# Kernel optimization log

Hardware: AMD Instinct MI355X
Metric: run time of the kernel (lower is better)

The kernel has to match this reference:

```python
import jax, jax.numpy as jnp
import numpy as np

N = 100000      # nodes
E = 1600000     # edges (avg degree 16)
F_IN = 128      # num_node_features
H = 128         # hidden_size
C = 64          # num_classes


def sage_conv(x, src, dst, W_l, W_r, b, num_nodes):
    """PyG SAGEConv (mean aggr): out = lin_l(mean_{j->i} x_j) + lin_r(x_i) + b."""
    msg = x[src]                                                  # [E, F] gather
    agg = jax.ops.segment_sum(msg, dst, num_segments=num_nodes)   # [N, F] scatter-add
    deg = jax.ops.segment_sum(jnp.ones((src.shape[0],), x.dtype), dst,
                              num_segments=num_nodes)             # [N]
    agg = agg / jnp.maximum(deg, 1.0)[:, None]                    # mean (safe for isolated nodes)
    return agg @ W_l + x @ W_r + b


def setup_inputs() -> dict:
    key = jax.random.key(0)
    ks = jax.random.split(key, 8)
    x = jax.random.normal(ks[0], (N, F_IN), dtype=jnp.float32)
    edge_index = jax.random.randint(ks[1], (2, E), 0, N, dtype=jnp.int32).astype(jnp.int64)
    W1_l = jax.random.normal(ks[2], (F_IN, H), dtype=jnp.float32) / np.float32(np.sqrt(F_IN))
    W1_r = jax.random.normal(ks[3], (F_IN, H), dtype=jnp.float32) / np.float32(np.sqrt(F_IN))
    b1 = jnp.zeros((H,), jnp.float32)
    W2_l = jax.random.normal(ks[4], (H, C), dtype=jnp.float32) / np.float32(np.sqrt(H))
    W2_r = jax.random.normal(ks[5], (H, C), dtype=jnp.float32) / np.float32(np.sqrt(H))
    b2 = jnp.zeros((C,), jnp.float32)
    return {"x": x, "edge_index": edge_index,
            "W1_l": W1_l, "W1_r": W1_r, "b1": b1,
            "W2_l": W2_l, "W2_r": W2_r, "b2": b2}


def reference(x, edge_index, W1_l, W1_r, b1, W2_l, W2_r, b2):
    src, dst = edge_index[0], edge_index[1]
    h = jax.nn.relu(sage_conv(x, src, dst, W1_l, W1_r, b1, N))   # dropout: eval mode => identity
    logits = sage_conv(h, src, dst, W2_l, W2_r, b2, N)
    return jax.nn.log_softmax(logits, axis=1)
```

## Files before the change

### kernel.cpp

```cpp
#include <hip/hip_runtime.h>

#define Nn 100000
#define Ee 1600000
#define FIN 128
#define HID 128
#define CLS 64
#define NB 196
#define BCAP 9216

typedef unsigned short ushort_t;
typedef unsigned char uchar_t;
typedef unsigned int uint_t;
typedef __attribute__((ext_vector_type(8))) short bf16x8;
typedef __attribute__((ext_vector_type(4))) float f32x4;
typedef __attribute__((ext_vector_type(2))) float f32x2;

__device__ __forceinline__ ushort_t f2bf(float f) {
    uint_t u = __float_as_uint(f);
    return (ushort_t)((u + 0x7fffu + ((u >> 16) & 1u)) >> 16);
}
__device__ __forceinline__ float bflo(uint_t u) { return __uint_as_float(u << 16); }
__device__ __forceinline__ float bfhi(uint_t u) { return __uint_as_float(u & 0xffff0000u); }


__global__ __launch_bounds__(1024) void k_front(const int* __restrict__ src,
                                                const int* __restrict__ dst,
                                                int* __restrict__ bcur,
                                                uint2* __restrict__ bedge,
                                                const float* __restrict__ x,
                                                ushort_t* __restrict__ xb,
                                                uint_t* __restrict__ xq,
                                                const float* __restrict__ W1l,
                                                const float* __restrict__ W1r,
                                                const float* __restrict__ W2l,
                                                const float* __restrict__ W2r,
                                                ushort_t* __restrict__ w1lt,
                                                ushort_t* __restrict__ w1rt,
                                                ushort_t* __restrict__ w2lt,
                                                ushort_t* __restrict__ w2rt) {
    __shared__ int h[NB];
    __shared__ int lbase[NB];
    int b = blockIdx.x;
    int t = threadIdx.x;
    if (b < NB) {
        if (t < NB) h[t] = 0;
        __syncthreads();
        int base = b * 8192;
        int bk[8], loc[8];
        #pragma unroll
        for (int it = 0; it < 8; ++it) {
            int e = base + it * 1024 + t;
            if (e < Ee) {
                bk[it] = dst[e] >> 9;
                loc[it] = atomicAdd(&h[bk[it]], 1);
            }
        }
        __syncthreads();
        if (t < NB && h[t]) lbase[t] = atomicAdd(&bcur[t], h[t]);
        __syncthreads();
        #pragma unroll
        for (int it = 0; it < 8; ++it) {
            int e = base + it * 1024 + t;
            if (e < Ee) {
                int pos = lbase[bk[it]] + loc[it];
                if (pos < BCAP)
                    bedge[(size_t)bk[it] * BCAP + pos] = make_uint2((uint_t)src[e], (uint_t)dst[e]);
            }
        }
    } else if (b < NB + 3125) {
        int i = (b - NB) * 1024 + t;
        float4 v = reinterpret_cast<const float4*>(x)[i];
        ushort4 o;
        o.x = f2bf(v.x); o.y = f2bf(v.y); o.z = f2bf(v.z); o.w = f2bf(v.w);
        reinterpret_cast<ushort4*>(xb)[i] = o;
        int q = __builtin_amdgcn_cvt_pk_fp8_f32(v.x, v.y, 0, false);
        q = __builtin_amdgcn_cvt_pk_fp8_f32(v.z, v.w, q, true);
        xq[i] = (uint_t)q;
    } else {
        int j = b - (NB + 3125);
        const float* Wsrc; ushort_t* Wdst; int Ncols; int cb;
        if (j < 16)      { Wsrc = W1l; Wdst = w1lt; Ncols = 128; cb = j; }
        else if (j < 32) { Wsrc = W1r; Wdst = w1rt; Ncols = 128; cb = j - 16; }
        else if (j < 40) { Wsrc = W2l; Wdst = w2lt; Ncols = 64;  cb = j - 32; }
        else             { Wsrc = W2r; Wdst = w2rt; Ncols = 64;  cb = j - 40; }
        int i = cb * 1024 + t;
        if (i < 128 * Ncols) {
            int k = i / Ncols, n = i % Ncols;
            Wdst[(size_t)n * 128 + k] = f2bf(Wsrc[i]);
        }
    }
}

__global__ __launch_bounds__(1024) void k_fillB(const uint2* __restrict__ bedge,
                                                const int* __restrict__ bcur,
                                                int* __restrict__ rowptr,
                                                int* __restrict__ csr) {
    __shared__ int h[512];
    __shared__ int off[512];
    __shared__ int sbase;
    int b = blockIdx.x, t = threadIdx.x;
    if (t < 256) off[t] = (t < NB) ? min(bcur[t], BCAP) : 0;
    __syncthreads();
    for (int o = 1; o < 256; o <<= 1) {
        int v = (t < 256 && t >= o) ? off[t - o] : 0;
        __syncthreads();
        if (t < 256) off[t] += v;
        __syncthreads();
    }
    if (t == 0) sbase = off[b] - min(bcur[b], BCAP);
    if (b == NB - 1 && t == 0) rowptr[Nn] = off[NB - 1];
    __syncthreads();
    int base_ = sbase;
    int n = min(bcur[b], BCAP);
    int node0 = b << 9;
    const uint2* be = bedge + (size_t)b * BCAP;
    if (t < 512) h[t] = 0;
    __syncthreads();
    for (int i = t; i < n; i += 1024)
        atomicAdd(&h[(int)be[i].y - node0], 1);
    __syncthreads();
    if (t < 512) off[t] = h[t];
    __syncthreads();
    for (int o = 1; o < 512; o <<= 1) {
        int v = (t < 512 && t >= o) ? off[t - o] : 0;
        __syncthreads();
        if (t < 512) off[t] += v;
        __syncthreads();
    }
    if (t < 512) {
        int excl = off[t] - h[t];
        int node = node0 + t;
        if (node < Nn) rowptr[node] = base_ + excl;
        h[t] = excl;
    }
    __syncthreads();
    for (int i = t; i < n; i += 1024) {
        uint2 ed = be[i];
        int loc = atomicAdd(&h[(int)ed.y - node0], 1);
        csr[base_ + loc] = (int)ed.x;
    }
}


__global__ __launch_bounds__(256) void k_agg1(const uchar_t* __restrict__ xq,
                                              const int* __restrict__ rowptr,
                                              const int* __restrict__ csr,
                                              ushort_t* __restrict__ outb) {
    int wid = (blockIdx.x * blockDim.x + threadIdx.x) >> 6;
    int lane = threadIdx.x & 63;
    if (wid >= Nn) return;
    int s0 = __builtin_amdgcn_readfirstlane(rowptr[wid]);
    int s1 = __builtin_amdgcn_readfirstlane(rowptr[wid + 1]);
    float ax = 0.f, ay = 0.f;
    int e = s0;
    for (; e + 16 <= s1; e += 16) {
        int idx[16];
        #pragma unroll
        for (int j = 0; j < 16; ++j) idx[j] = __builtin_amdgcn_readfirstlane(csr[e + j]);
        ushort_t u[16];
        #pragma unroll
        for (int j = 0; j < 16; ++j)
            u[j] = *reinterpret_cast<const ushort_t*>(xq + (size_t)idx[j] * 128 + lane * 2);
        #pragma unroll
        for (int j = 0; j < 16; ++j) {
            f32x2 f = __builtin_amdgcn_cvt_pk_f32_fp8((int)u[j], false);
            ax += f.x; ay += f.y;
        }
    }
    for (; e + 8 <= s1; e += 8) {
        int idx[8];
        #pragma unroll
        for (int j = 0; j < 8; ++j) idx[j] = __builtin_amdgcn_readfirstlane(csr[e + j]);
        ushort_t u[8];
        #pragma unroll
        for (int j = 0; j < 8; ++j)
            u[j] = *reinterpret_cast<const ushort_t*>(xq + (size_t)idx[j] * 128 + lane * 2);
        #pragma unroll
        for (int j = 0; j < 8; ++j) {
            f32x2 f = __builtin_amdgcn_cvt_pk_f32_fp8((int)u[j], false);
            ax += f.x; ay += f.y;
        }
    }
    for (; e < s1; ++e) {
        int s = __builtin_amdgcn_readfirstlane(csr[e]);
        ushort_t u = *reinterpret_cast<const ushort_t*>(xq + (size_t)s * 128 + lane * 2);
        f32x2 f = __builtin_amdgcn_cvt_pk_f32_fp8((int)u, false);
        ax += f.x; ay += f.y;
    }
    float invd = (s1 > s0) ? 1.0f / (float)(s1 - s0) : 0.0f;
    uint_t o = (uint_t)f2bf(ax * invd) | ((uint_t)f2bf(ay * invd) << 16);
    *reinterpret_cast<uint_t*>(outb + (size_t)wid * 128 + lane * 2) = o;
}


__global__ __launch_bounds__(512) void k_gemm12(const ushort_t* __restrict__ Ab0,
                                                const ushort_t* __restrict__ Ab1,
                                                const ushort_t* __restrict__ Wt0,
                                                const ushort_t* __restrict__ Wt1,
                                                const float* __restrict__ b1,
                                                const ushort_t* __restrict__ Wtl,
                                                const ushort_t* __restrict__ Wtr,
                                                uchar_t* __restrict__ tb8,
                                                float* __restrict__ outu) {
    __shared__ char lwc[2 * 32768];
    const int tid = threadIdx.x;
    #pragma unroll
    for (int i = 0; i < 8; ++i) {
        int c = tid + i * 512;
        int pair = c >> 11;
        int col = (c & 2047) >> 4;
        int kc = c & 15;
        const ushort_t* Wsrc = pair ? Wt1 : Wt0;
        uint4 v = *reinterpret_cast<const uint4*>(Wsrc + col * 128 + kc * 8);
        int dst = ((pair << 15) | (col << 8) | (kc << 4)) ^ ((col & 7) << 4);
        *reinterpret_cast<uint4*>(lwc + dst) = v;
    }
    __syncthreads();

    int wid = tid >> 6;
    int gw = blockIdx.x * 8 + wid;
    int lane = tid & 63;
    int r = lane & 15;
    int kg = lane >> 4;
    bool active = (gw < Nn / 16);
    int row0 = gw * 16;

    f32x4 acc[8];
    #pragma unroll
    for (int c = 0; c < 8; ++c) acc[c] = (f32x4){0.f, 0.f, 0.f, 0.f};
    if (active) {
        #pragma unroll
        for (int pair = 0; pair < 2; ++pair) {
            const ushort_t* A = pair ? Ab1 : Ab0;
            #pragma unroll
            for (int ks = 0; ks < 4; ++ks) {
                int kbase = ks * 32 + kg * 8;
                bf16x8 af = *reinterpret_cast<const bf16x8*>(A + (size_t)(row0 + r) * 128 + kbase);
                #pragma unroll
                for (int c = 0; c < 8; ++c) {
                    int boff = ((pair << 15) | ((c * 16 + r) << 8) | (ks * 64 + kg * 16))
                               ^ ((r & 7) << 4);
                    bf16x8 bf = *reinterpret_cast<const bf16x8*>(lwc + boff);
                    acc[c] = __builtin_amdgcn_mfma_f32_16x16x32_bf16(af, bf, acc[c], 0, 0, 0);
                }
            }
        }
    }
    __syncthreads();

    if (active) {
        #pragma unroll
        for (int c = 0; c < 8; ++c) {
            float bv = b1[c * 16 + r];
            #pragma unroll
            for (int i = 0; i < 4; ++i) {
                int rl = wid * 16 + kg * 4 + i;
                int ha = ((rl << 8) | ((c * 16 + r) << 1)) ^ ((rl & 7) << 4);
                *reinterpret_cast<ushort_t*>(lwc + ha) = f2bf(fmaxf(acc[c][i] + bv, 0.f));
            }
        }
    }
    __syncthreads();
    if (!active) return;

    f32x4 accL[4], accR[4];
    #pragma unroll
    for (int c = 0; c < 4; ++c) {
        accL[c] = (f32x4){0.f, 0.f, 0.f, 0.f};
        accR[c] = (f32x4){0.f, 0.f, 0.f, 0.f};
    }
    #pragma unroll
    for (int ks = 0; ks < 4; ++ks) {
        int kbase = ks * 32 + kg * 8;
        int rl = wid * 16 + r;
        int ra = ((rl << 8) | (kbase << 1)) ^ ((r & 7) << 4);
        bf16x8 af = *reinterpret_cast<const bf16x8*>(lwc + ra);
        #pragma unroll
        for (int c = 0; c < 4; ++c) {
            bf16x8 bl = *reinterpret_cast<const bf16x8*>(Wtl + (size_t)(c * 16 + r) * 128 + kbase);
            accL[c] = __builtin_amdgcn_mfma_f32_16x16x32_bf16(af, bl, accL[c], 0, 0, 0);
            bf16x8 br = *reinterpret_cast<const bf16x8*>(Wtr + (size_t)(c * 16 + r) * 128 + kbase);
            accR[c] = __builtin_amdgcn_mfma_f32_16x16x32_bf16(af, br, accR[c], 0, 0, 0);
        }
    }
    #pragma unroll
    for (int c = 0; c < 4; ++c) {
        #pragma unroll
        for (int i = 0; i < 4; ++i) {
            int row = row0 + kg * 4 + i;
            int q = __builtin_amdgcn_cvt_pk_fp8_f32(accL[c][i], accL[c][i], 0, false);
            tb8[(size_t)row * 64 + c * 16 + r] = (uchar_t)(q & 0xff);
            outu[(size_t)row * 64 + c * 16 + r] = accR[c][i];
        }
    }
}


__global__ __launch_bounds__(256) void k_logsm(float* __restrict__ out,
                                               const uchar_t* __restrict__ tb8,
                                               const int* __restrict__ rowptr,
                                               const int* __restrict__ csr,
                                               const float* __restrict__ bias) {
    int wid = (blockIdx.x * blockDim.x + threadIdx.x) >> 6;
    int lane = threadIdx.x & 63;
    if (wid >= Nn) return;
    int s0 = __builtin_amdgcn_readfirstlane(rowptr[wid]);
    int s1 = __builtin_amdgcn_readfirstlane(rowptr[wid + 1]);
    float a = 0.f;
    int e = s0;
    for (; e + 16 <= s1; e += 16) {
        int idx[16];
        #pragma unroll
        for (int j = 0; j < 16; ++j) idx[j] = __builtin_amdgcn_readfirstlane(csr[e + j]);
        uchar_t u[16];
        #pragma unroll
        for (int j = 0; j < 16; ++j) u[j] = tb8[(size_t)idx[j] * 64 + lane];
        #pragma unroll
        for (int j = 0; j < 16; ++j) a += __builtin_amdgcn_cvt_f32_fp8((int)u[j], 0);
    }
    for (; e + 8 <= s1; e += 8) {
        int idx[8];
        #pragma unroll
        for (int j = 0; j < 8; ++j) idx[j] = __builtin_amdgcn_readfirstlane(csr[e + j]);
        uchar_t u[8];
        #pragma unroll
        for (int j = 0; j < 8; ++j) u[j] = tb8[(size_t)idx[j] * 64 + lane];
        #pragma unroll
        for (int j = 0; j < 8; ++j) a += __builtin_amdgcn_cvt_f32_fp8((int)u[j], 0);
    }
    for (; e < s1; ++e) {
        int s = __builtin_amdgcn_readfirstlane(csr[e]);
        a += __builtin_amdgcn_cvt_f32_fp8((int)tb8[(size_t)s * 64 + lane], 0);
    }
    float invd = (s1 > s0) ? 1.0f / (float)(s1 - s0) : 0.0f;
    size_t o = (size_t)wid * 64 + lane;
    float v = (out[o] + a * invd) + bias[lane];
    float m = v;
    #pragma unroll
    for (int off = 32; off; off >>= 1) m = fmaxf(m, __shfl_xor(m, off));
    float ex = __expf(v - m);
    float s_ = ex;
    #pragma unroll
    for (int off = 32; off; off >>= 1) s_ += __shfl_xor(s_, off);
    out[o] = v - m - __logf(s_);
}


extern "C" void kernel_launch(void* const* d_in, const int* in_sizes, int n_in,
                              void* d_out, int out_size, void* d_ws, size_t ws_size,
                              hipStream_t stream) {
    const float* x   = (const float*)d_in[0];
    const int*   ei  = (const int*)d_in[1];
    const float* W1l = (const float*)d_in[2];
    const float* W1r = (const float*)d_in[3];
    const float* b1  = (const float*)d_in[4];
    const float* W2l = (const float*)d_in[5];
    const float* W2r = (const float*)d_in[6];
    const float* b2  = (const float*)d_in[7];
    float* out = (float*)d_out;

    char* ws = (char*)d_ws;
    int*      rowptr = (int*)(ws + 800768);
    int*      csr    = (int*)(ws + 1201152);
    ushort_t* xb     = (ushort_t*)(ws + 7601152);
    ushort_t* aggb   = (ushort_t*)(ws + 33201152);
    ushort_t* w1lt   = (ushort_t*)(ws + 58801152);
    ushort_t* w1rt   = (ushort_t*)(ws + 58833920);
    ushort_t* w2lt   = (ushort_t*)(ws + 58866688);
    ushort_t* w2rt   = (ushort_t*)(ws + 58883072);
    uint2*    bedge  = (uint2*)(ws + 60000000);
    int*      bcur   = (int*)(ws + 74450688);
    uint_t*   xq     = (uint_t*)(ws + 74451968);
    uchar_t*  tb8    = (uchar_t*)(ws + 87252992);

    const int* src = ei;
    const int* dst = ei + Ee;

    hipMemsetAsync(bcur, 0, NB * 4, stream);

    k_front<<<NB + 3125 + 48, 1024, 0, stream>>>(src, dst, bcur, bedge, x, xb, xq,
                                                 W1l, W1r, W2l, W2r,
                                                 w1lt, w1rt, w2lt, w2rt);
    k_fillB<<<NB, 1024, 0, stream>>>(bedge, bcur, rowptr, csr);

    k_agg1<<<(Nn + 3) / 4, 256, 0, stream>>>((const uchar_t*)xq, rowptr, csr, aggb);

    k_gemm12<<<(Nn / 16 + 7) / 8, 512, 0, stream>>>(aggb, xb, w1lt, w1rt, b1,
                                                    w2lt, w2rt, tb8, out);

    k_logsm<<<(Nn + 3) / 4, 256, 0, stream>>>(out, tb8, rowptr, csr, b2);
}
```

Before: 191.3 us.

## Split wavefront into four edge groups with wide per-lane gathers in aggregation kernels

Both neighbor-aggregation kernels now split each 64-lane wavefront into four 16-lane groups. Each group gathers a different neighbor row with a wide vector load (8 bytes or 4 bytes per lane instead of 2 or 1), then the partial sums are combined with cross-lane shuffles. The intent is fewer, wider memory instructions and more neighbor rows in flight per wavefront, while keeping the dependent CSR index loads uniform. In exchange it adds shuffle reductions, a masked tail path and lower lane utilisation on the final store. The log-softmax reductions are also narrowed to 16-lane shuffles over four values per lane.

Result: faster. 177.3 us, median of 2 (-7.3%).

```diff
diff --git a/kernel.cpp b/kernel.cpp
--- a/kernel.cpp
+++ b/kernel.cpp
@@ -151,45 +151,76 @@
     if (wid >= Nn) return;
     int s0 = __builtin_amdgcn_readfirstlane(rowptr[wid]);
     int s1 = __builtin_amdgcn_readfirstlane(rowptr[wid + 1]);
-    float ax = 0.f, ay = 0.f;
+    int g = lane >> 4;
+    int col = lane & 15;
+    const uchar_t* base = xq + col * 8;
+    float a0 = 0.f, a1 = 0.f, a2 = 0.f, a3 = 0.f;
+    float a4 = 0.f, a5 = 0.f, a6 = 0.f, a7 = 0.f;
     int e = s0;
     for (; e + 16 <= s1; e += 16) {
-        int idx[16];
-        #pragma unroll
-        for (int j = 0; j < 16; ++j) idx[j] = __builtin_amdgcn_readfirstlane(csr[e + j]);
-        ushort_t u[16];
-        #pragma unroll
-        for (int j = 0; j < 16; ++j)
-            u[j] = *reinterpret_cast<const ushort_t*>(xq + (size_t)idx[j] * 128 + lane * 2);
-        #pragma unroll
-        for (int j = 0; j < 16; ++j) {
-            f32x2 f = __builtin_amdgcn_cvt_pk_f32_fp8((int)u[j], false);
-            ax += f.x; ay += f.y;
-        }
-    }
-    for (; e + 8 <= s1; e += 8) {
-        int idx[8];
-        #pragma unroll
-        for (int j = 0; j < 8; ++j) idx[j] = __builtin_amdgcn_readfirstlane(csr[e + j]);
-        ushort_t u[8];
-        #pragma unroll
-        for (int j = 0; j < 8; ++j)
-            u[j] = *reinterpret_cast<const ushort_t*>(xq + (size_t)idx[j] * 128 + lane * 2);
-        #pragma unroll
-        for (int j = 0; j < 8; ++j) {
-            f32x2 f = __builtin_amdgcn_cvt_pk_f32_fp8((int)u[j], false);
-            ax += f.x; ay += f.y;
-        }
-    }
-    for (; e < s1; ++e) {
-        int s = __builtin_amdgcn_readfirstlane(csr[e]);
-        ushort_t u = *reinterpret_cast<const ushort_t*>(xq + (size_t)s * 128 + lane * 2);
-        f32x2 f = __builtin_amdgcn_cvt_pk_f32_fp8((int)u, false);
-        ax += f.x; ay += f.y;
-    }
-    float invd = (s1 > s0) ? 1.0f / (float)(s1 - s0) : 0.0f;
-    uint_t o = (uint_t)f2bf(ax * invd) | ((uint_t)f2bf(ay * invd) << 16);
-    *reinterpret_cast<uint_t*>(outb + (size_t)wid * 128 + lane * 2) = o;
+        #pragma unroll
+        for (int q = 0; q < 4; ++q) {
+            int i0 = __builtin_amdgcn_readfirstlane(csr[e + q * 4 + 0]);
+            int i1 = __builtin_amdgcn_readfirstlane(csr[e + q * 4 + 1]);
+            int i2 = __builtin_amdgcn_readfirstlane(csr[e + q * 4 + 2]);
+            int i3 = __builtin_amdgcn_readfirstlane(csr[e + q * 4 + 3]);
+            int id = (g & 2) ? ((g & 1) ? i3 : i2) : ((g & 1) ? i1 : i0);
+            uint2 u = *reinterpret_cast<const uint2*>(base + (size_t)id * 128);
+            f32x2 f0 = __builtin_amdgcn_cvt_pk_f32_fp8((int)u.x, false);
+            f32x2 f1 = __builtin_amdgcn_cvt_pk_f32_fp8((int)u.x, true);
+            f32x2 f2 = __builtin_amdgcn_cvt_pk_f32_fp8((int)u.y, false);
+            f32x2 f3 = __builtin_amdgcn_cvt_pk_f32_fp8((int)u.y, true);
+            a0 += f0.x; a1 += f0.y; a2 += f1.x; a3 += f1.y;
+            a4 += f2.x; a5 += f2.y; a6 += f3.x; a7 += f3.y;
+        }
+    }
+    for (; e + 4 <= s1; e += 4) {
+        int i0 = __builtin_amdgcn_readfirstlane(csr[e + 0]);
+        int i1 = __builtin_amdgcn_readfirstlane(csr[e + 1]);
+        int i2 = __builtin_amdgcn_readfirstlane(csr[e + 2]);
+        int i3 = __builtin_amdgcn_readfirstlane(csr[e + 3]);
+        int id = (g & 2) ? ((g & 1) ? i3 : i2) : ((g & 1) ? i1 : i0);
+        uint2 u = *reinterpret_cast<const uint2*>(base + (size_t)id * 128);
+        f32x2 f0 = __builtin_amdgcn_cvt_pk_f32_fp8((int)u.x, false);
+        f32x2 f1 = __builtin_amdgcn_cvt_pk_f32_fp8((int)u.x, true);
+        f32x2 f2 = __builtin_amdgcn_cvt_pk_f32_fp8((int)u.y, false);
+        f32x2 f3 = __builtin_amdgcn_cvt_pk_f32_fp8((int)u.y, true);
+        a0 += f0.x; a1 += f0.y; a2 += f1.x; a3 += f1.y;
+        a4 += f2.x; a5 += f2.y; a6 += f3.x; a7 += f3.y;
+    }
+    int rem = s1 - e;
+    if (rem > 0) {
+        int i0 = __builtin_amdgcn_readfirstlane(csr[e]);
+        int i1 = __builtin_amdgcn_readfirstlane(csr[min(e + 1, s1 - 1)]);
+        int i2 = __builtin_amdgcn_readfirstlane(csr[min(e + 2, s1 - 1)]);
+        int id = (g & 2) ? i2 : ((g & 1) ? i1 : i0);
+        if (g < rem) {
+            uint2 u = *reinterpret_cast<const uint2*>(base + (size_t)id * 128);
+            f32x2 f0 = __builtin_amdgcn_cvt_pk_f32_fp8((int)u.x, false);
+            f32x2 f1 = __builtin_amdgcn_cvt_pk_f32_fp8((int)u.x, true);
+            f32x2 f2 = __builtin_amdgcn_cvt_pk_f32_fp8((int)u.y, false);
+            f32x2 f3 = __builtin_amdgcn_cvt_pk_f32_fp8((int)u.y, true);
+            a0 += f0.x; a1 += f0.y; a2 += f1.x; a3 += f1.y;
+            a4 += f2.x; a5 += f2.y; a6 += f3.x; a7 += f3.y;
+        }
+    }
+    a0 += __shfl_xor(a0, 16); a0 += __shfl_xor(a0, 32);
+    a1 += __shfl_xor(a1, 16); a1 += __shfl_xor(a1, 32);
+    a2 += __shfl_xor(a2, 16); a2 += __shfl_xor(a2, 32);
+    a3 += __shfl_xor(a3, 16); a3 += __shfl_xor(a3, 32);
+    a4 += __shfl_xor(a4, 16); a4 += __shfl_xor(a4, 32);
+    a5 += __shfl_xor(a5, 16); a5 += __shfl_xor(a5, 32);
+    a6 += __shfl_xor(a6, 16); a6 += __shfl_xor(a6, 32);
+    a7 += __shfl_xor(a7, 16); a7 += __shfl_xor(a7, 32);
+    if (g == 0) {
+        float invd = (s1 > s0) ? 1.0f / (float)(s1 - s0) : 0.0f;
+        uint4 o;
+        o.x = (uint_t)f2bf(a0 * invd) | ((uint_t)f2bf(a1 * invd) << 16);
+        o.y = (uint_t)f2bf(a2 * invd) | ((uint_t)f2bf(a3 * invd) << 16);
+        o.z = (uint_t)f2bf(a4 * invd) | ((uint_t)f2bf(a5 * invd) << 16);
+        o.w = (uint_t)f2bf(a6 * invd) | ((uint_t)f2bf(a7 * invd) << 16);
+        *reinterpret_cast<uint4*>(outb + (size_t)wid * 128 + col * 8) = o;
+    }
 }
 
 
@@ -306,43 +337,73 @@
     if (wid >= Nn) return;
     int s0 = __builtin_amdgcn_readfirstlane(rowptr[wid]);
     int s1 = __builtin_amdgcn_readfirstlane(rowptr[wid + 1]);
-    float a = 0.f;
+    int g = lane >> 4;
+    int col = lane & 15;
+    const uchar_t* base = tb8 + col * 4;
+    float4 uo = *reinterpret_cast<const float4*>(out + (size_t)wid * 64 + col * 4);
+    float4 bv = *reinterpret_cast<const float4*>(bias + col * 4);
+    float a0 = 0.f, a1 = 0.f, a2 = 0.f, a3 = 0.f;
     int e = s0;
     for (; e + 16 <= s1; e += 16) {
-        int idx[16];
-        #pragma unroll
-        for (int j = 0; j < 16; ++j) idx[j] = __builtin_amdgcn_readfirstlane(csr[e + j]);
-        uchar_t u[16];
-        #pragma unroll
-        for (int j = 0; j < 16; ++j) u[j] = tb8[(size_t)idx[j] * 64 + lane];
-        #pragma unroll
-        for (int j = 0; j < 16; ++j) a += __builtin_amdgcn_cvt_f32_fp8((int)u[j], 0);
-    }
-    for (; e + 8 <= s1; e += 8) {
-        int idx[8];
-        #pragma unroll
-        for (int j = 0; j < 8; ++j) idx[j] = __builtin_amdgcn_readfirstlane(csr[e + j]);
-        uchar_t u[8];
-        #pragma unroll
-        for (int j = 0; j < 8; ++j) u[j] = tb8[(size_t)idx[j] * 64 + lane];
-        #pragma unroll
-        for (int j = 0; j < 8; ++j) a += __builtin_amdgcn_cvt_f32_fp8((int)u[j], 0);
-    }
-    for (; e < s1; ++e) {
-        int s = __builtin_amdgcn_readfirstlane(csr[e]);
-        a += __builtin_amdgcn_cvt_f32_fp8((int)tb8[(size_t)s * 64 + lane], 0);
-    }
+        #pragma unroll
+        for (int q = 0; q < 4; ++q) {
+            int i0 = __builtin_amdgcn_readfirstlane(csr[e + q * 4 + 0]);
+            int i1 = __builtin_amdgcn_readfirstlane(csr[e + q * 4 + 1]);
+            int i2 = __builtin_amdgcn_readfirstlane(csr[e + q * 4 + 2]);
+            int i3 = __builtin_amdgcn_readfirstlane(csr[e + q * 4 + 3]);
+            int id = (g & 2) ? ((g & 1) ? i3 : i2) : ((g & 1) ? i1 : i0);
+            uint_t u = *reinterpret_cast<const uint_t*>(base + (size_t)id * 64);
+            f32x2 f0 = __builtin_amdgcn_cvt_pk_f32_fp8((int)u, false);
+            f32x2 f1 = __builtin_amdgcn_cvt_pk_f32_fp8((int)u, true);
+            a0 += f0.x; a1 += f0.y; a2 += f1.x; a3 += f1.y;
+        }
+    }
+    for (; e + 4 <= s1; e += 4) {
+        int i0 = __builtin_amdgcn_readfirstlane(csr[e + 0]);
+        int i1 = __builtin_amdgcn_readfirstlane(csr[e + 1]);
+        int i2 = __builtin_amdgcn_readfirstlane(csr[e + 2]);
+        int i3 = __builtin_amdgcn_readfirstlane(csr[e + 3]);
+        int id = (g & 2) ? ((g & 1) ? i3 : i2) : ((g & 1) ? i1 : i0);
+        uint_t u = *reinterpret_cast<const uint_t*>(base + (size_t)id * 64);
+        f32x2 f0 = __builtin_amdgcn_cvt_pk_f32_fp8((int)u, false);
+        f32x2 f1 = __builtin_amdgcn_cvt_pk_f32_fp8((int)u, true);
+        a0 += f0.x; a1 += f0.y; a2 += f1.x; a3 += f1.y;
+    }
+    int rem = s1 - e;
+    if (rem > 0) {
+        int i0 = __builtin_amdgcn_readfirstlane(csr[e]);
+        int i1 = __builtin_amdgcn_readfirstlane(csr[min(e + 1, s1 - 1)]);
+        int i2 = __builtin_amdgcn_readfirstlane(csr[min(e + 2, s1 - 1)]);
+        int id = (g & 2) ? i2 : ((g & 1) ? i1 : i0);
+        if (g < rem) {
+            uint_t u = *reinterpret_cast<const uint_t*>(base + (size_t)id * 64);
+            f32x2 f0 = __builtin_amdgcn_cvt_pk_f32_fp8((int)u, false);
+            f32x2 f1 = __builtin_amdgcn_cvt_pk_f32_fp8((int)u, true);
+            a0 += f0.x; a1 += f0.y; a2 += f1.x; a3 += f1.y;
+        }
+    }
+    a0 += __shfl_xor(a0, 16); a0 += __shfl_xor(a0, 32);
+    a1 += __shfl_xor(a1, 16); a1 += __shfl_xor(a1, 32);
+    a2 += __shfl_xor(a2, 16); a2 += __shfl_xor(a2, 32);
+    a3 += __shfl_xor(a3, 16); a3 += __shfl_xor(a3, 32);
     float invd = (s1 > s0) ? 1.0f / (float)(s1 - s0) : 0.0f;
-    size_t o = (size_t)wid * 64 + lane;
-    float v = (out[o] + a * invd) + bias[lane];
-    float m = v;
-    #pragma unroll
-    for (int off = 32; off; off >>= 1) m = fmaxf(m, __shfl_xor(m, off));
-    float ex = __expf(v - m);
-    float s_ = ex;
-    #pragma unroll
-    for (int off = 32; off; off >>= 1) s_ += __shfl_xor(s_, off);
-    out[o] = v - m - __logf(s_);
+    float v0 = (uo.x + a0 * invd) + bv.x;
+    float v1 = (uo.y + a1 * invd) + bv.y;
+    float v2 = (uo.z + a2 * invd) + bv.z;
+    float v3 = (uo.w + a3 * invd) + bv.w;
+    float m = fmaxf(fmaxf(v0, v1), fmaxf(v2, v3));
+    #pragma unroll
+    for (int off = 8; off; off >>= 1) m = fmaxf(m, __shfl_xor(m, off));
+    float s_ = __expf(v0 - m) + __expf(v1 - m) + __expf(v2 - m) + __expf(v3 - m);
+    #pragma unroll
+    for (int off = 8; off; off >>= 1) s_ += __shfl_xor(s_, off);
+    float ls = __logf(s_);
+    if (g == 0) {
+        float4 o;
+        o.x = v0 - m - ls; o.y = v1 - m - ls;
+        o.z = v2 - m - ls; o.w = v3 - m - ls;
+        *reinterpret_cast<float4*>(out + (size_t)wid * 64 + col * 4) = o;
+    }
 }
 
 
```
